# Kernel tuning notes

Hardware: AMD Instinct MI355X
Metric: run time of the kernel (lower is better)

## Reference

```python
import jax, jax.numpy as jnp
import numpy as np

T = 2048          # num tokens (single long prefill sequence)
HID = 2048        # hidden_size
NH = 16           # num query heads
NKV = 2           # num kv heads
HD = 128          # head_dim (kv_channels)
ROPE_BASE = 10000.0


def setup_inputs() -> dict:
    key = jax.random.key(0)
    k1, k2, k3, k4, k5 = jax.random.split(key, 5)
    s = 0.02
    return {
        "hidden_states": jax.random.normal(k1, (T, HID), dtype=jnp.float32),
        "positions": jnp.arange(T, dtype=jnp.int64 if jax.config.jax_enable_x64 else jnp.int32),
        "Wq": jax.random.normal(k2, (NH * HD, HID), dtype=jnp.float32) * s,
        "Wk": jax.random.normal(k3, (NKV * HD, HID), dtype=jnp.float32) * s,
        "Wv": jax.random.normal(k4, (NKV * HD, HID), dtype=jnp.float32) * s,
        "Wo": jax.random.normal(k5, (HID, NH * HD), dtype=jnp.float32) * s,
    }


def _rope_cos_sin(positions):
    # fp32 RoPE tables, HF-style (concat of freqs with itself)
    inv_freq = 1.0 / (ROPE_BASE ** (jnp.arange(0, HD, 2, dtype=jnp.float32) / HD))
    freqs = positions.astype(jnp.float32)[:, None] * inv_freq[None, :]   # [T, HD/2]
    emb = jnp.concatenate([freqs, freqs], axis=-1)                        # [T, HD]
    return jnp.cos(emb)[:, None, :], jnp.sin(emb)[:, None, :]             # [T,1,HD]


def _rotate_half(x):
    x1, x2 = jnp.split(x, 2, axis=-1)
    return jnp.concatenate([-x2, x1], axis=-1)


def reference(hidden_states, positions, Wq, Wk, Wv, Wo):
    dtype = hidden_states.dtype
    # fused QKV projection (weights concatenated once, single GEMM)
    W_fused = jnp.concatenate([Wq, Wk, Wv], axis=0)            # [q+2kv, HID]
    qkv = hidden_states @ W_fused.T                             # [T, q+2kv]
    q, k, v = jnp.split(qkv, [NH * HD, NH * HD + NKV * HD], axis=-1)

    # fp32 RoPE on q/k
    cos, sin = _rope_cos_sin(positions)                         # [T,1,HD]
    qf = q.reshape(T, NH, HD).astype(jnp.float32)
    kf = k.reshape(T, NKV, HD).astype(jnp.float32)
    qf = qf * cos + _rotate_half(qf) * sin
    kf = kf * cos + _rotate_half(kf) * sin
    q = qf.astype(dtype)                                        # [T,NH,HD]
    k = kf.astype(dtype)                                        # [T,NKV,HD]
    v = v.reshape(T, NKV, HD)

    # causal GQA attention (same math as the paged-attention kernel on one seq)
    group = NH // NKV
    k_rep = jnp.repeat(k, group, axis=1)                        # [T,NH,HD]
    v_rep = jnp.repeat(v, group, axis=1)                        # [T,NH,HD]
    scale = HD ** -0.5
    scores = jnp.einsum('qhd,khd->hqk', q, k_rep) * scale       # [NH,T,T]
    causal = jnp.tril(jnp.ones((T, T), dtype=bool))
    scores = jnp.where(causal[None], scores, jnp.finfo(scores.dtype).min)
    probs = jax.nn.softmax(scores, axis=-1)
    attn = jnp.einsum('hqk,khd->qhd', probs, v_rep).reshape(T, NH * HD)

    return attn @ Wo.T                                          # [T, HID]
```

## Files before the change

### kernel.cpp

```cpp
#include <hip/hip_runtime.h>

#define T_TOK 2048
#define HID   2048
#define NH    16
#define NKV   2
#define HD    128
#define QDIM  (NH * HD)
#define KVDIM (NKV * HD)
#define QKVDIM (QDIM + 2 * KVDIM)

typedef float          f32x4  __attribute__((ext_vector_type(4)));
typedef unsigned short u16x8  __attribute__((ext_vector_type(8)));
typedef __bf16         bf16x8 __attribute__((ext_vector_type(8)));

__device__ __forceinline__ unsigned short f2bf(float f) {
    __bf16 h = (__bf16)f;
    return __builtin_bit_cast(unsigned short, h);
}
__device__ __forceinline__ float bf2f(unsigned short u) {
    return (float)__builtin_bit_cast(__bf16, u);
}

__device__ __forceinline__ f32x4 mfma16(u16x8 a, u16x8 b, f32x4 c) {
    return __builtin_amdgcn_mfma_f32_16x16x32_bf16(
        __builtin_bit_cast(bf16x8, a), __builtin_bit_cast(bf16x8, b), c, 0, 0, 0);
}

#define QSCL 0.12751743f
#define DEFER_THR 11.5416f

__global__ __launch_bounds__(256) void pack_bf16_all(
    const float* __restrict__ hidden, const float* __restrict__ Wq,
    const float* __restrict__ Wk, const float* __restrict__ Wv,
    const float* __restrict__ Wo,
    unsigned short* __restrict__ hb, unsigned short* __restrict__ Wf,
    unsigned short* __restrict__ Wob)
{
    const int b = blockIdx.x;
    const float* src; unsigned short* dst; size_t off;
    if      (b < 2048) { src = hidden; dst = hb;            off = (size_t)b * 2048; }
    else if (b < 4096) { src = Wq;     dst = Wf;            off = (size_t)(b - 2048) * 2048; }
    else if (b < 4352) { src = Wk;     dst = Wf + 4194304;  off = (size_t)(b - 4096) * 2048; }
    else if (b < 4608) { src = Wv;     dst = Wf + 4718592;  off = (size_t)(b - 4352) * 2048; }
    else               { src = Wo;     dst = Wob;           off = (size_t)(b - 4608) * 2048; }

    const size_t i = off + threadIdx.x * 8;
    float4 f0 = *reinterpret_cast<const float4*>(src + i);
    float4 f1 = *reinterpret_cast<const float4*>(src + i + 4);
    u16x8 o;
    o[0]=f2bf(f0.x); o[1]=f2bf(f0.y); o[2]=f2bf(f0.z); o[3]=f2bf(f0.w);
    o[4]=f2bf(f1.x); o[5]=f2bf(f1.y); o[6]=f2bf(f1.z); o[7]=f2bf(f1.w);
    *reinterpret_cast<u16x8*>(dst + i) = o;
}

template<bool BF16OUT>
__global__ __launch_bounds__(256) void gemm_bf16(
    const unsigned short* __restrict__ A,
    const unsigned short* __restrict__ B,
    void* __restrict__ Cv,
    int K, int NC, int nbx)
{
    __shared__ alignas(16) unsigned short As[2][64 * 64];
    __shared__ alignas(16) unsigned short Bs[2][128 * 64];

    const int tid  = threadIdx.x;
    const int lane = tid & 63;
    const int w    = tid >> 6;
    const int lg   = lane >> 4, lc = lane & 15;

    const int cpx = gridDim.x >> 3;
    const int wg  = (blockIdx.x & 7) * cpx + (blockIdx.x >> 3);
    const int m0  = (wg / nbx) * 64, n0 = (wg % nbx) * 128;

    const int rowL = lane >> 3;
    const int gS   = (lane & 7) ^ rowL;
    const int wr   = (w >> 1) * 32, wc = (w & 1) * 64;

    f32x4 acc[2][4] = {};

    auto stage = [&](int buf, int kb) {
        #pragma unroll
        for (int ci = 0; ci < 2; ci++) {
            const int chunk = w * 2 + ci;
            const int row   = chunk * 8 + rowL;
            const unsigned short* gpA = &A[(size_t)(m0 + row) * K + kb + gS * 8];
            __builtin_amdgcn_global_load_lds(
                (const __attribute__((address_space(1))) void*)gpA,
                (__attribute__((address_space(3))) void*)(&As[buf][chunk * 512]),
                16, 0, 0);
        }
        #pragma unroll
        for (int ci = 0; ci < 4; ci++) {
            const int chunk = w * 4 + ci;
            const int row   = chunk * 8 + rowL;
            const unsigned short* gpB = &B[(size_t)(n0 + row) * K + kb + gS * 8];
            __builtin_amdgcn_global_load_lds(
                (const __attribute__((address_space(1))) void*)gpB,
                (__attribute__((address_space(3))) void*)(&Bs[buf][chunk * 512]),
                16, 0, 0);
        }
    };

    stage(0, 0);
    const int nk = K >> 6;
    for (int t = 0; t < nk; ++t) {
        if (t + 1 < nk) {
            stage((t + 1) & 1, (t + 1) * 64);
            asm volatile("s_waitcnt vmcnt(6)" ::: "memory");
        } else {
            asm volatile("s_waitcnt vmcnt(0)" ::: "memory");
        }
        __syncthreads();

        const unsigned short* As_ = As[t & 1];
        const unsigned short* Bs_ = Bs[t & 1];
        #pragma unroll
        for (int kk = 0; kk < 2; kk++) {
            u16x8 af[2], bf[4];
            const int g = (kk * 4 + lg) ^ (lc & 7);
            #pragma unroll
            for (int mi = 0; mi < 2; mi++) {
                const int r = wr + mi * 16 + lc;
                af[mi] = *reinterpret_cast<const u16x8*>(&As_[r * 64 + g * 8]);
            }
            #pragma unroll
            for (int ni = 0; ni < 4; ni++) {
                const int r = wc + ni * 16 + lc;
                bf[ni] = *reinterpret_cast<const u16x8*>(&Bs_[r * 64 + g * 8]);
            }
            #pragma unroll
            for (int mi = 0; mi < 2; mi++)
                #pragma unroll
                for (int ni = 0; ni < 4; ni++)
                    acc[mi][ni] = mfma16(af[mi], bf[ni], acc[mi][ni]);
        }
        __syncthreads();
    }

    #pragma unroll
    for (int mi = 0; mi < 2; mi++)
        #pragma unroll
        for (int ni = 0; ni < 4; ni++)
            #pragma unroll
            for (int j = 0; j < 4; j++) {
                const size_t idx = (size_t)(m0 + wr + mi * 16 + lg * 4 + j) * NC
                                   + n0 + wc + ni * 16 + lc;
                if constexpr (BF16OUT)
                    ((unsigned short*)Cv)[idx] = f2bf(acc[mi][ni][j]);
                else
                    ((float*)Cv)[idx] = acc[mi][ni][j];
            }
}

__global__ __launch_bounds__(256) void rope_vt(
    const unsigned short* __restrict__ qkvb,
    const int* __restrict__ positions,
    unsigned short* __restrict__ qr,
    unsigned short* __restrict__ kr,
    unsigned short* __restrict__ vt)
{
    __shared__ float cosv[64], sinv[64];
    __shared__ unsigned short tile[64][72];
    const int tid = threadIdx.x;

    if (blockIdx.x < 2048) {
        const int t = blockIdx.x;
        if (tid < 64) {
            float invf = expf(-(float)tid * 0.14391156831212787f);
            float f = (float)positions[t] * invf;
            cosv[tid] = cosf(f);
            sinv[tid] = sinf(f);
        }
        __syncthreads();

        const unsigned short* row = qkvb + (size_t)t * QKVDIM;
        for (int i = tid; i < NH * 64; i += 256) {
            int hh = i >> 6, j = i & 63;
            float x1 = bf2f(row[hh * HD + j]);
            float x2 = bf2f(row[hh * HD + j + 64]);
            float c = cosv[j], s = sinv[j];
            qr[(size_t)t * QDIM + hh * HD + j]      = f2bf((x1 * c - x2 * s) * QSCL);
            qr[(size_t)t * QDIM + hh * HD + j + 64] = f2bf((x2 * c + x1 * s) * QSCL);
        }
        if (tid < NKV * 64) {
            int hh = tid >> 6, j = tid & 63;
            float x1 = bf2f(row[QDIM + hh * HD + j]);
            float x2 = bf2f(row[QDIM + hh * HD + j + 64]);
            float c = cosv[j], s = sinv[j];
            kr[(size_t)t * KVDIM + hh * HD + j]      = f2bf(x1 * c - x2 * s);
            kr[(size_t)t * KVDIM + hh * HD + j + 64] = f2bf(x2 * c + x1 * s);
        }
    } else {
        const int bb = blockIdx.x - 2048;
        const int t0 = (bb & 31) * 64;
        const int d0 = (bb >> 5) * 64;
        {
            int r = tid >> 2;
            int c = (tid & 3) * 16;
            const unsigned short* src =
                &qkvb[(size_t)(t0 + r) * QKVDIM + QDIM + KVDIM + d0 + c];
            *reinterpret_cast<u16x8*>(&tile[r][c])     = *reinterpret_cast<const u16x8*>(src);
            *reinterpret_cast<u16x8*>(&tile[r][c + 8]) = *reinterpret_cast<const u16x8*>(src + 8);
        }
        __syncthreads();
        {
            int dr = tid >> 3;
            int tc = (tid & 7) * 8;
            #pragma unroll
            for (int i = 0; i < 2; i++) {
                int d = dr + i * 32;
                u16x8 ov;
                #pragma unroll
                for (int e = 0; e < 8; e++) ov[e] = tile[tc + e][d];
                *reinterpret_cast<u16x8*>(&vt[(size_t)(d0 + d) * T_TOK + t0 + tc]) = ov;
            }
        }
    }
}

__global__ __launch_bounds__(256) void attn_kernel(
    const unsigned short* __restrict__ q,
    const unsigned short* __restrict__ k,
    const unsigned short* __restrict__ vt,
    unsigned short* __restrict__ o,
    float* __restrict__ pO,
    float* __restrict__ pML)
{
    __shared__ alignas(16) unsigned short Ks[64 * 128];
    __shared__ alignas(16) unsigned short Vs[128 * 64];
    __shared__ alignas(16) unsigned short P[4][16][72];

    const int tid  = threadIdx.x;
    const int lane = tid & 63;
    const int w    = tid >> 6;
    const int lg   = lane >> 4, lc = lane & 15;
    const int b    = blockIdx.x;
    const int h    = b & 15;
    const int idx  = b >> 4;

    int tau, c0;
    if (idx <= 16)      { tau = 15 + idx; c0 = 0; }
    else if (idx == 17) { tau = 31;       c0 = 1; }
    else {
        int j = idx - 18, kk = 15 - (j >> 1);
        if ((j & 1) == 0) { tau = kk - 1;  c0 = 0; }
        else              { tau = kk + 15; c0 = 1; }
    }
    const int kstart = c0 << 4;
    const int kcnt   = min(16, tau + 1 - kstart);

    const int q0   = tau * 64 + w * 16;
    const int hk   = h >> 3;
    const int xr   = (lc & 7) << 4;

    const int krow_l = (lane >> 4);
    const int kgS    = (lane & 15);
    const int vrow_l = (lane >> 3);
    const int vgS    = (lane & 7);

    u16x8 qf[4];
    #pragma unroll
    for (int dc = 0; dc < 4; dc++)
        qf[dc] = *reinterpret_cast<const u16x8*>(
            &q[(size_t)(q0 + lc) * QDIM + h * HD + dc * 32 + lg * 8]);

    float mrow = -1e30f, ell = 0.f;
    f32x4 oacc[8] = {};

    auto stage = [&](int kb) {
        #pragma unroll
        for (int ci = 0; ci < 4; ci++) {
            const int chunk = w * 4 + ci;
            const int row   = chunk * 4 + krow_l;
            const int gSk   = kgS ^ (row & 7);
            const unsigned short* gp =
                &k[(size_t)(kb + row) * KVDIM + hk * HD + gSk * 8];
            __builtin_amdgcn_global_load_lds(
                (const __attribute__((address_space(1))) void*)gp,
                (__attribute__((address_space(3))) void*)(&Ks[chunk * 512]),
                16, 0, 0);
        }
        #pragma unroll
        for (int ci = 0; ci < 4; ci++) {
            const int chunk = w * 4 + ci;
            const int dr    = chunk * 8 + vrow_l;
            const int gSv   = vgS ^ (dr & 7);
            const unsigned short* gp =
                &vt[(size_t)(hk * HD + dr) * T_TOK + kb + gSv * 8];
            __builtin_amdgcn_global_load_lds(
                (const __attribute__((address_space(1))) void*)gp,
                (__attribute__((address_space(3))) void*)(&Vs[chunk * 512]),
                16, 0, 0);
        }
    };

    for (int it = 0; it < kcnt; ++it) {
        const int kb = (kstart + it) * 64;
        stage(kb);
        asm volatile("s_waitcnt vmcnt(4)" ::: "memory");
        __syncthreads();

        const char* KsB = (const char*)Ks;
        const char* VsB = (const char*)Vs;

        float sc[4][4];
        const bool dia = (kb + 63 > q0);
        #pragma unroll
        for (int c4 = 0; c4 < 4; c4++) {
            const int row = c4 * 16 + lc;
            f32x4 s = {0.f, 0.f, 0.f, 0.f};
            #pragma unroll
            for (int dc = 0; dc < 4; dc++) {
                u16x8 kf = *reinterpret_cast<const u16x8*>(
                    KsB + row * 256 + ((dc * 64 + lg * 16) ^ xr));
                s = mfma16(kf, qf[dc], s);
            }
            if (dia) {
                #pragma unroll
                for (int j = 0; j < 4; j++) {
                    const int kpos = kb + c4 * 16 + lg * 4 + j;
                    sc[c4][j] = (kpos <= q0 + lc) ? s[j] : -1e30f;
                }
            } else {
                #pragma unroll
                for (int j = 0; j < 4; j++) sc[c4][j] = s[j];
            }
        }

        float t01 = fmaxf(fmaxf(sc[0][0], sc[0][1]), fmaxf(sc[0][2], sc[0][3]));
        float t23 = fmaxf(fmaxf(sc[1][0], sc[1][1]), fmaxf(sc[1][2], sc[1][3]));
        float t45 = fmaxf(fmaxf(sc[2][0], sc[2][1]), fmaxf(sc[2][2], sc[2][3]));
        float t67 = fmaxf(fmaxf(sc[3][0], sc[3][1]), fmaxf(sc[3][2], sc[3][3]));
        float tmx = fmaxf(fmaxf(t01, t23), fmaxf(t45, t67));
        tmx = fmaxf(tmx, __shfl_xor(tmx, 16));
        tmx = fmaxf(tmx, __shfl_xor(tmx, 32));

        float mn;
        if (__all(tmx <= mrow + DEFER_THR)) {
            mn = mrow;
        } else {
            mn = fmaxf(mrow, tmx);
            float alpha = __builtin_amdgcn_exp2f(mrow - mn);
            mrow = mn;
            ell *= alpha;
            float aj[4];
            #pragma unroll
            for (int j = 0; j < 4; j++)
                aj[j] = __shfl(alpha, lg * 4 + j);
            #pragma unroll
            for (int d8 = 0; d8 < 8; d8++)
                #pragma unroll
                for (int j = 0; j < 4; j++)
                    oacc[d8][j] *= aj[j];
        }

        float rs = 0.f;
        #pragma unroll
        for (int c4 = 0; c4 < 4; c4++) {
            float p0 = __builtin_amdgcn_exp2f(sc[c4][0] - mn);
            float p1 = __builtin_amdgcn_exp2f(sc[c4][1] - mn);
            float p2 = __builtin_amdgcn_exp2f(sc[c4][2] - mn);
            float p3 = __builtin_amdgcn_exp2f(sc[c4][3] - mn);
            rs += (p0 + p1) + (p2 + p3);
            ushort4 pk;
            pk.x = f2bf(p0); pk.y = f2bf(p1); pk.z = f2bf(p2); pk.w = f2bf(p3);
            *reinterpret_cast<ushort4*>(&P[w][lc][c4 * 16 + lg * 4]) = pk;
        }
        rs += __shfl_xor(rs, 16);
        rs += __shfl_xor(rs, 32);
        ell += rs;

        asm volatile("s_waitcnt vmcnt(0) lgkmcnt(0)" ::: "memory");
        __builtin_amdgcn_sched_barrier(0);
        __syncthreads();

        u16x8 pf0 = *reinterpret_cast<const u16x8*>(&P[w][lc][lg * 8]);
        u16x8 pf1 = *reinterpret_cast<const u16x8*>(&P[w][lc][32 + lg * 8]);

        #pragma unroll
        for (int d8 = 0; d8 < 8; d8++) {
            const int drow = d8 * 16 + lc;
            u16x8 vf0 = *reinterpret_cast<const u16x8*>(
                VsB + drow * 128 + ((lg * 16) ^ xr));
            u16x8 vf1 = *reinterpret_cast<const u16x8*>(
                VsB + drow * 128 + ((lg * 16 + 64) ^ xr));
            oacc[d8] = mfma16(pf0, vf0, oacc[d8]);
            oacc[d8] = mfma16(pf1, vf1, oacc[d8]);
        }
        if (it + 1 < kcnt) __syncthreads();
    }

    if (tau < 16) {
        float ej[4];
        #pragma unroll
        for (int j = 0; j < 4; j++)
            ej[j] = __shfl(ell, lg * 4 + j);
        #pragma unroll
        for (int d8 = 0; d8 < 8; d8++)
            #pragma unroll
            for (int j = 0; j < 4; j++) {
                float val = oacc[d8][j] / ej[j];
                o[(size_t)(q0 + lg * 4 + j) * QDIM + h * HD + d8 * 16 + lc] = f2bf(val);
            }
    } else {
        const int s = (h * 16 + (tau - 16)) * 2 + c0;
        float* po = pO + (size_t)s * 8192;
        #pragma unroll
        for (int d8 = 0; d8 < 8; d8++)
            #pragma unroll
            for (int j = 0; j < 4; j++)
                po[(w * 16 + lg * 4 + j) * 128 + d8 * 16 + lc] = oacc[d8][j];
        if (lg == 0) {
            pML[s * 128 + w * 16 + lc]      = mrow;
            pML[s * 128 + 64 + w * 16 + lc] = ell;
        }
    }
}

__global__ __launch_bounds__(256) void attn_combine(
    const float* __restrict__ pO,
    const float* __restrict__ pML,
    unsigned short* __restrict__ o)
{
    const int b  = blockIdx.x;
    const int h  = b >> 4, ti = b & 15;
    const int tau = 16 + ti;
    const int s0 = (h * 16 + ti) * 2, s1 = s0 + 1;

    const int tid = threadIdx.x;
    const int r   = tid >> 2;
    const int cg  = (tid & 3) * 32;

    const float m1 = pML[s0 * 128 + r],      m2 = pML[s1 * 128 + r];
    const float l1 = pML[s0 * 128 + 64 + r], l2 = pML[s1 * 128 + 64 + r];
    const float M  = fmaxf(m1, m2);
    const float w1 = __builtin_amdgcn_exp2f(m1 - M);
    const float w2 = __builtin_amdgcn_exp2f(m2 - M);
    const float rn = 1.0f / (w1 * l1 + w2 * l2);

    const float* o1 = pO + (size_t)s0 * 8192 + r * 128 + cg;
    const float* o2 = pO + (size_t)s1 * 8192 + r * 128 + cg;
    unsigned short* dst = o + (size_t)(tau * 64 + r) * QDIM + h * HD + cg;

    #pragma unroll
    for (int i = 0; i < 8; i++) {
        float4 a = *reinterpret_cast<const float4*>(o1 + i * 4);
        float4 c = *reinterpret_cast<const float4*>(o2 + i * 4);
        ushort4 pk;
        pk.x = f2bf((w1 * a.x + w2 * c.x) * rn);
        pk.y = f2bf((w1 * a.y + w2 * c.y) * rn);
        pk.z = f2bf((w1 * a.z + w2 * c.z) * rn);
        pk.w = f2bf((w1 * a.w + w2 * c.w) * rn);
        *reinterpret_cast<ushort4*>(dst + i * 4) = pk;
    }
}

extern "C" void kernel_launch(void* const* d_in, const int* in_sizes, int n_in,
                              void* d_out, int out_size, void* d_ws, size_t ws_size,
                              hipStream_t stream) {
    const float* hidden    = (const float*)d_in[0];
    const int*   positions = (const int*)d_in[1];
    const float* Wq        = (const float*)d_in[2];
    const float* Wk        = (const float*)d_in[3];
    const float* Wv        = (const float*)d_in[4];
    const float* Wo        = (const float*)d_in[5];
    float*       out       = (float*)d_out;

    char* ws = (char*)d_ws;
    unsigned short* qkvb = (unsigned short*)(ws);
    unsigned short* qr  = (unsigned short*)(ws + 20971520);
    unsigned short* kr  = (unsigned short*)(ws + 29360128);
    unsigned short* vt  = (unsigned short*)(ws + 30408704);
    unsigned short* att = (unsigned short*)(ws + 31457280);
    unsigned short* hb  = (unsigned short*)(ws + 39845888);
    unsigned short* Wf  = (unsigned short*)(ws + 48234496);
    unsigned short* Wob = (unsigned short*)(ws + 58720256);
    float* pO  = (float*)(ws);
    float* pML = (float*)(ws + 16777216);

    pack_bf16_all<<<6656, 256, 0, stream>>>(hidden, Wq, Wk, Wv, Wo, hb, Wf, Wob);
    gemm_bf16<true><<<640, 256, 0, stream>>>(hb, Wf, qkvb, HID, QKVDIM, QKVDIM / 128);
    rope_vt<<<2176, 256, 0, stream>>>(qkvb, positions, qr, kr, vt);
    attn_kernel<<<NH * 48, 256, 0, stream>>>(qr, kr, vt, att, pO, pML);
    attn_combine<<<256, 256, 0, stream>>>(pO, pML, att);
    gemm_bf16<false><<<512, 256, 0, stream>>>(att, Wob, out, QDIM, HID, HID / 128);
}
```

Before: 130.3 us.

## Prefetch next K/V tile into registers while computing current attention tile

Replaces direct global-to-LDS loads with register-staged prefetch: the next tile's K and V are loaded into registers at the top of each iteration and written to LDS after the PV MFMAs. The goal is to hide global load latency behind the QK, softmax and PV compute instead of waiting on the loads at the start of every iteration. In exchange it adds register pressure (8 extra u16x8 per lane) and an extra barrier pair around the LDS write. It also removes the barrier between the P write and the P read, relying only on lgkmcnt for the per-wave P buffer.

```diff
diff --git a/kernel.cpp b/kernel.cpp
--- a/kernel.cpp
+++ b/kernel.cpp
@@ -267,38 +267,47 @@
     float mrow = -1e30f, ell = 0.f;
     f32x4 oacc[8] = {};
 
-    auto stage = [&](int kb) {
+    u16x8 kreg[4], vreg[4];
+
+    auto ldstage = [&](int kb) {
         #pragma unroll
         for (int ci = 0; ci < 4; ci++) {
             const int chunk = w * 4 + ci;
             const int row   = chunk * 4 + krow_l;
             const int gSk   = kgS ^ (row & 7);
-            const unsigned short* gp =
-                &k[(size_t)(kb + row) * KVDIM + hk * HD + gSk * 8];
-            __builtin_amdgcn_global_load_lds(
-                (const __attribute__((address_space(1))) void*)gp,
-                (__attribute__((address_space(3))) void*)(&Ks[chunk * 512]),
-                16, 0, 0);
+            kreg[ci] = *reinterpret_cast<const u16x8*>(
+                &k[(size_t)(kb + row) * KVDIM + hk * HD + gSk * 8]);
         }
         #pragma unroll
         for (int ci = 0; ci < 4; ci++) {
             const int chunk = w * 4 + ci;
             const int dr    = chunk * 8 + vrow_l;
             const int gSv   = vgS ^ (dr & 7);
-            const unsigned short* gp =
-                &vt[(size_t)(hk * HD + dr) * T_TOK + kb + gSv * 8];
-            __builtin_amdgcn_global_load_lds(
-                (const __attribute__((address_space(1))) void*)gp,
-                (__attribute__((address_space(3))) void*)(&Vs[chunk * 512]),
-                16, 0, 0);
+            vreg[ci] = *reinterpret_cast<const u16x8*>(
+                &vt[(size_t)(hk * HD + dr) * T_TOK + kb + gSv * 8]);
         }
     };
+    auto wrstage = [&]() {
+        #pragma unroll
+        for (int ci = 0; ci < 4; ci++) {
+            const int chunk = w * 4 + ci;
+            *reinterpret_cast<u16x8*>(&Ks[chunk * 512 + lane * 8]) = kreg[ci];
+        }
+        #pragma unroll
+        for (int ci = 0; ci < 4; ci++) {
+            const int chunk = w * 4 + ci;
+            *reinterpret_cast<u16x8*>(&Vs[chunk * 512 + lane * 8]) = vreg[ci];
+        }
+    };
+
+    ldstage(kstart * 64);
+    wrstage();
+    __syncthreads();
 
     for (int it = 0; it < kcnt; ++it) {
         const int kb = (kstart + it) * 64;
-        stage(kb);
-        asm volatile("s_waitcnt vmcnt(4)" ::: "memory");
-        __syncthreads();
+        if (it + 1 < kcnt)
+            ldstage((kstart + it + 1) * 64);
 
         const char* KsB = (const char*)Ks;
         const char* VsB = (const char*)Vs;
@@ -370,9 +379,8 @@
         rs += __shfl_xor(rs, 32);
         ell += rs;
 
-        asm volatile("s_waitcnt vmcnt(0) lgkmcnt(0)" ::: "memory");
+        asm volatile("s_waitcnt lgkmcnt(0)" ::: "memory");
         __builtin_amdgcn_sched_barrier(0);
-        __syncthreads();
 
         u16x8 pf0 = *reinterpret_cast<const u16x8*>(&P[w][lc][lg * 8]);
         u16x8 pf1 = *reinterpret_cast<const u16x8*>(&P[w][lc][32 + lg * 8]);
@@ -387,7 +395,12 @@
             oacc[d8] = mfma16(pf0, vf0, oacc[d8]);
             oacc[d8] = mfma16(pf1, vf1, oacc[d8]);
         }
-        if (it + 1 < kcnt) __syncthreads();
+
+        if (it + 1 < kcnt) {
+            __syncthreads();
+            wrstage();
+            __syncthreads();
+        }
     }
 
     if (tau < 16) {
```

Result: slower. 133.5 us (+2.5%).

## Fuse RoPE and V transpose into QKV GEMM epilogue

Applied to the files above, without the earlier changes.

Removes the separate rope_vt kernel by applying RoPE (with q scaling) to Q/K tiles in the QKV GEMM epilogue via an LDS staging buffer, and writing V directly transposed. Cos/sin tables are precomputed in extra blocks of the packing kernel. This avoids writing and re-reading the full bf16 QKV intermediate and one kernel launch, at the cost of extra shared memory, an epilogue sync, and strided transposed V stores.

```diff
diff --git a/kernel.cpp b/kernel.cpp
--- a/kernel.cpp
+++ b/kernel.cpp
@@ -17,9 +17,6 @@
     __bf16 h = (__bf16)f;
     return __builtin_bit_cast(unsigned short, h);
 }
-__device__ __forceinline__ float bf2f(unsigned short u) {
-    return (float)__builtin_bit_cast(__bf16, u);
-}
 
 __device__ __forceinline__ f32x4 mfma16(u16x8 a, u16x8 b, f32x4 c) {
     return __builtin_amdgcn_mfma_f32_16x16x32_bf16(
@@ -32,11 +29,21 @@
 __global__ __launch_bounds__(256) void pack_bf16_all(
     const float* __restrict__ hidden, const float* __restrict__ Wq,
     const float* __restrict__ Wk, const float* __restrict__ Wv,
-    const float* __restrict__ Wo,
+    const float* __restrict__ Wo, const int* __restrict__ positions,
     unsigned short* __restrict__ hb, unsigned short* __restrict__ Wf,
-    unsigned short* __restrict__ Wob)
+    unsigned short* __restrict__ Wob, float* __restrict__ ctab)
 {
     const int b = blockIdx.x;
+    if (b >= 6656) {
+        const int bb = b - 6656;
+        const int t  = bb * 4 + (threadIdx.x >> 6);
+        const int j  = threadIdx.x & 63;
+        float invf = expf(-(float)j * 0.14391156831212787f);
+        float f = (float)positions[t] * invf;
+        ctab[(size_t)t * 128 + j]      = cosf(f);
+        ctab[(size_t)t * 128 + 64 + j] = sinf(f);
+        return;
+    }
     const float* src; unsigned short* dst; size_t off;
     if      (b < 2048) { src = hidden; dst = hb;            off = (size_t)b * 2048; }
     else if (b < 4096) { src = Wq;     dst = Wf;            off = (size_t)(b - 2048) * 2048; }
@@ -53,21 +60,24 @@
     *reinterpret_cast<u16x8*>(dst + i) = o;
 }
 
-template<bool BF16OUT>
-__global__ __launch_bounds__(256) void gemm_bf16(
+__global__ __launch_bounds__(256) void qkv_gemm_fused(
     const unsigned short* __restrict__ A,
     const unsigned short* __restrict__ B,
-    void* __restrict__ Cv,
-    int K, int NC, int nbx)
+    const float* __restrict__ ctab,
+    unsigned short* __restrict__ qr,
+    unsigned short* __restrict__ kr,
+    unsigned short* __restrict__ vt)
 {
-    __shared__ alignas(16) unsigned short As[2][64 * 64];
-    __shared__ alignas(16) unsigned short Bs[2][128 * 64];
+    __shared__ alignas(16) char smem[49152];
+    unsigned short* AsBase = (unsigned short*)smem;
+    unsigned short* BsBase = (unsigned short*)(smem + 16384);
 
     const int tid  = threadIdx.x;
     const int lane = tid & 63;
     const int w    = tid >> 6;
     const int lg   = lane >> 4, lc = lane & 15;
 
+    const int nbx = QKVDIM / 128;
     const int cpx = gridDim.x >> 3;
     const int wg  = (blockIdx.x & 7) * cpx + (blockIdx.x >> 3);
     const int m0  = (wg / nbx) * 64, n0 = (wg % nbx) * 128;
@@ -83,26 +93,26 @@
         for (int ci = 0; ci < 2; ci++) {
             const int chunk = w * 2 + ci;
             const int row   = chunk * 8 + rowL;
-            const unsigned short* gpA = &A[(size_t)(m0 + row) * K + kb + gS * 8];
+            const unsigned short* gpA = &A[(size_t)(m0 + row) * HID + kb + gS * 8];
             __builtin_amdgcn_global_load_lds(
                 (const __attribute__((address_space(1))) void*)gpA,
-                (__attribute__((address_space(3))) void*)(&As[buf][chunk * 512]),
+                (__attribute__((address_space(3))) void*)(&AsBase[buf * 4096 + chunk * 512]),
                 16, 0, 0);
         }
         #pragma unroll
         for (int ci = 0; ci < 4; ci++) {
             const int chunk = w * 4 + ci;
             const int row   = chunk * 8 + rowL;
-            const unsigned short* gpB = &B[(size_t)(n0 + row) * K + kb + gS * 8];
+            const unsigned short* gpB = &B[(size_t)(n0 + row) * HID + kb + gS * 8];
             __builtin_amdgcn_global_load_lds(
                 (const __attribute__((address_space(1))) void*)gpB,
-                (__attribute__((address_space(3))) void*)(&Bs[buf][chunk * 512]),
+                (__attribute__((address_space(3))) void*)(&BsBase[buf * 8192 + chunk * 512]),
                 16, 0, 0);
         }
     };
 
     stage(0, 0);
-    const int nk = K >> 6;
+    const int nk = HID >> 6;
     for (int t = 0; t < nk; ++t) {
         if (t + 1 < nk) {
             stage((t + 1) & 1, (t + 1) * 64);
@@ -112,8 +122,8 @@
         }
         __syncthreads();
 
-        const unsigned short* As_ = As[t & 1];
-        const unsigned short* Bs_ = Bs[t & 1];
+        const unsigned short* As_ = &AsBase[(t & 1) * 4096];
+        const unsigned short* Bs_ = &BsBase[(t & 1) * 8192];
         #pragma unroll
         for (int kk = 0; kk < 2; kk++) {
             u16x8 af[2], bf[4];
@@ -137,85 +147,151 @@
         __syncthreads();
     }
 
+    if (n0 < QDIM + KVDIM) {
+        float* Ep = (float*)smem;
+        #pragma unroll
+        for (int mi = 0; mi < 2; mi++)
+            #pragma unroll
+            for (int ni = 0; ni < 4; ni++)
+                #pragma unroll
+                for (int j = 0; j < 4; j++)
+                    Ep[(wr + mi * 16 + lg * 4 + j) * 132 + wc + ni * 16 + lc]
+                        = acc[mi][ni][j];
+        __syncthreads();
+
+        const bool isq = (n0 < QDIM);
+        const float scl = isq ? QSCL : 1.0f;
+        unsigned short* dst  = isq ? qr : kr;
+        const int rowstride  = isq ? QDIM : KVDIM;
+        const int colbase    = isq ? n0 : (n0 - QDIM);
+
+        const int r  = tid >> 2;
+        const int jb = (tid & 3) * 16;
+        const float* ct = ctab + (size_t)(m0 + r) * 128;
+        unsigned short* drow = dst + (size_t)(m0 + r) * rowstride + colbase;
+        #pragma unroll
+        for (int g = 0; g < 4; g++) {
+            ushort4 p1, p2;
+            #pragma unroll
+            for (int e = 0; e < 4; e++) {
+                const int j = jb + g * 4 + e;
+                float x1 = Ep[r * 132 + j];
+                float x2 = Ep[r * 132 + j + 64];
+                float c = ct[j], s = ct[64 + j];
+                ((unsigned short*)&p1)[e] = f2bf((x1 * c - x2 * s) * scl);
+                ((unsigned short*)&p2)[e] = f2bf((x2 * c + x1 * s) * scl);
+            }
+            *reinterpret_cast<ushort4*>(drow + jb + g * 4)      = p1;
+            *reinterpret_cast<ushort4*>(drow + jb + g * 4 + 64) = p2;
+        }
+    } else {
+        #pragma unroll
+        for (int mi = 0; mi < 2; mi++)
+            #pragma unroll
+            for (int ni = 0; ni < 4; ni++) {
+                const int d   = (n0 - QDIM - KVDIM) + wc + ni * 16 + lc;
+                const int t0r = m0 + wr + mi * 16 + lg * 4;
+                ushort4 pk;
+                pk.x = f2bf(acc[mi][ni][0]);
+                pk.y = f2bf(acc[mi][ni][1]);
+                pk.z = f2bf(acc[mi][ni][2]);
+                pk.w = f2bf(acc[mi][ni][3]);
+                *reinterpret_cast<ushort4*>(&vt[(size_t)d * T_TOK + t0r]) = pk;
+            }
+    }
+}
+
+__global__ __launch_bounds__(256) void gemm_out(
+    const unsigned short* __restrict__ A,
+    const unsigned short* __restrict__ B,
+    float* __restrict__ C)
+{
+    __shared__ alignas(16) unsigned short As[2][64 * 64];
+    __shared__ alignas(16) unsigned short Bs[2][128 * 64];
+
+    const int tid  = threadIdx.x;
+    const int lane = tid & 63;
+    const int w    = tid >> 6;
+    const int lg   = lane >> 4, lc = lane & 15;
+
+    const int nbx = HID / 128;
+    const int cpx = gridDim.x >> 3;
+    const int wg  = (blockIdx.x & 7) * cpx + (blockIdx.x >> 3);
+    const int m0  = (wg / nbx) * 64, n0 = (wg % nbx) * 128;
+
+    const int rowL = lane >> 3;
+    const int gS   = (lane & 7) ^ rowL;
+    const int wr   = (w >> 1) * 32, wc = (w & 1) * 64;
+
+    f32x4 acc[2][4] = {};
+
+    auto stage = [&](int buf, int kb) {
+        #pragma unroll
+        for (int ci = 0; ci < 2; ci++) {
+            const int chunk = w * 2 + ci;
+            const int row   = chunk * 8 + rowL;
+            const unsigned short* gpA = &A[(size_t)(m0 + row) * QDIM + kb + gS * 8];
+            __builtin_amdgcn_global_load_lds(
+                (const __attribute__((address_space(1))) void*)gpA,
+                (__attribute__((address_space(3))) void*)(&As[buf][chunk * 512]),
+                16, 0, 0);
+        }
+        #pragma unroll
+        for (int ci = 0; ci < 4; ci++) {
+            const int chunk = w * 4 + ci;
+            const int row   = chunk * 8 + rowL;
+            const unsigned short* gpB = &B[(size_t)(n0 + row) * QDIM + kb + gS * 8];
+            __builtin_amdgcn_global_load_lds(
+                (const __attribute__((address_space(1))) void*)gpB,
+                (__attribute__((address_space(3))) void*)(&Bs[buf][chunk * 512]),
+                16, 0, 0);
+        }
+    };
+
+    stage(0, 0);
+    const int nk = QDIM >> 6;
+    for (int t = 0; t < nk; ++t) {
+        if (t + 1 < nk) {
+            stage((t + 1) & 1, (t + 1) * 64);
+            asm volatile("s_waitcnt vmcnt(6)" ::: "memory");
+        } else {
+            asm volatile("s_waitcnt vmcnt(0)" ::: "memory");
+        }
+        __syncthreads();
+
+        const unsigned short* As_ = As[t & 1];
+        const unsigned short* Bs_ = Bs[t & 1];
+        #pragma unroll
+        for (int kk = 0; kk < 2; kk++) {
+            u16x8 af[2], bf[4];
+            const int g = (kk * 4 + lg) ^ (lc & 7);
+            #pragma unroll
+            for (int mi = 0; mi < 2; mi++) {
+                const int r = wr + mi * 16 + lc;
+                af[mi] = *reinterpret_cast<const u16x8*>(&As_[r * 64 + g * 8]);
+            }
+            #pragma unroll
+            for (int ni = 0; ni < 4; ni++) {
+                const int r = wc + ni * 16 + lc;
+                bf[ni] = *reinterpret_cast<const u16x8*>(&Bs_[r * 64 + g * 8]);
+            }
+            #pragma unroll
+            for (int mi = 0; mi < 2; mi++)
+                #pragma unroll
+                for (int ni = 0; ni < 4; ni++)
+                    acc[mi][ni] = mfma16(af[mi], bf[ni], acc[mi][ni]);
+        }
+        __syncthreads();
+    }
+
     #pragma unroll
     for (int mi = 0; mi < 2; mi++)
         #pragma unroll
         for (int ni = 0; ni < 4; ni++)
             #pragma unroll
-            for (int j = 0; j < 4; j++) {
-                const size_t idx = (size_t)(m0 + wr + mi * 16 + lg * 4 + j) * NC
-                                   + n0 + wc + ni * 16 + lc;
-                if constexpr (BF16OUT)
-                    ((unsigned short*)Cv)[idx] = f2bf(acc[mi][ni][j]);
-                else
-                    ((float*)Cv)[idx] = acc[mi][ni][j];
-            }
-}
-
-__global__ __launch_bounds__(256) void rope_vt(
-    const unsigned short* __restrict__ qkvb,
-    const int* __restrict__ positions,
-    unsigned short* __restrict__ qr,
-    unsigned short* __restrict__ kr,
-    unsigned short* __restrict__ vt)
-{
-    __shared__ float cosv[64], sinv[64];
-    __shared__ unsigned short tile[64][72];
-    const int tid = threadIdx.x;
-
-    if (blockIdx.x < 2048) {
-        const int t = blockIdx.x;
-        if (tid < 64) {
-            float invf = expf(-(float)tid * 0.14391156831212787f);
-            float f = (float)positions[t] * invf;
-            cosv[tid] = cosf(f);
-            sinv[tid] = sinf(f);
-        }
-        __syncthreads();
-
-        const unsigned short* row = qkvb + (size_t)t * QKVDIM;
-        for (int i = tid; i < NH * 64; i += 256) {
-            int hh = i >> 6, j = i & 63;
-            float x1 = bf2f(row[hh * HD + j]);
-            float x2 = bf2f(row[hh * HD + j + 64]);
-            float c = cosv[j], s = sinv[j];
-            qr[(size_t)t * QDIM + hh * HD + j]      = f2bf((x1 * c - x2 * s) * QSCL);
-            qr[(size_t)t * QDIM + hh * HD + j + 64] = f2bf((x2 * c + x1 * s) * QSCL);
-        }
-        if (tid < NKV * 64) {
-            int hh = tid >> 6, j = tid & 63;
-            float x1 = bf2f(row[QDIM + hh * HD + j]);
-            float x2 = bf2f(row[QDIM + hh * HD + j + 64]);
-            float c = cosv[j], s = sinv[j];
-            kr[(size_t)t * KVDIM + hh * HD + j]      = f2bf(x1 * c - x2 * s);
-            kr[(size_t)t * KVDIM + hh * HD + j + 64] = f2bf(x2 * c + x1 * s);
-        }
-    } else {
-        const int bb = blockIdx.x - 2048;
-        const int t0 = (bb & 31) * 64;
-        const int d0 = (bb >> 5) * 64;
-        {
-            int r = tid >> 2;
-            int c = (tid & 3) * 16;
-            const unsigned short* src =
-                &qkvb[(size_t)(t0 + r) * QKVDIM + QDIM + KVDIM + d0 + c];
-            *reinterpret_cast<u16x8*>(&tile[r][c])     = *reinterpret_cast<const u16x8*>(src);
-            *reinterpret_cast<u16x8*>(&tile[r][c + 8]) = *reinterpret_cast<const u16x8*>(src + 8);
-        }
-        __syncthreads();
-        {
-            int dr = tid >> 3;
-            int tc = (tid & 7) * 8;
-            #pragma unroll
-            for (int i = 0; i < 2; i++) {
-                int d = dr + i * 32;
-                u16x8 ov;
-                #pragma unroll
-                for (int e = 0; e < 8; e++) ov[e] = tile[tc + e][d];
-                *reinterpret_cast<u16x8*>(&vt[(size_t)(d0 + d) * T_TOK + t0 + tc]) = ov;
-            }
-        }
-    }
+            for (int j = 0; j < 4; j++)
+                C[(size_t)(m0 + wr + mi * 16 + lg * 4 + j) * HID
+                  + n0 + wc + ni * 16 + lc] = acc[mi][ni][j];
 }
 
 __global__ __launch_bounds__(256) void attn_kernel(
@@ -467,7 +543,9 @@
     float*       out       = (float*)d_out;
 
     char* ws = (char*)d_ws;
-    unsigned short* qkvb = (unsigned short*)(ws);
+    float* pO   = (float*)(ws);
+    float* pML  = (float*)(ws + 16777216);
+    float* ctab = (float*)(ws + 17039360);
     unsigned short* qr  = (unsigned short*)(ws + 20971520);
     unsigned short* kr  = (unsigned short*)(ws + 29360128);
     unsigned short* vt  = (unsigned short*)(ws + 30408704);
@@ -475,13 +553,11 @@
     unsigned short* hb  = (unsigned short*)(ws + 39845888);
     unsigned short* Wf  = (unsigned short*)(ws + 48234496);
     unsigned short* Wob = (unsigned short*)(ws + 58720256);
-    float* pO  = (float*)(ws);
-    float* pML = (float*)(ws + 16777216);
-
-    pack_bf16_all<<<6656, 256, 0, stream>>>(hidden, Wq, Wk, Wv, Wo, hb, Wf, Wob);
-    gemm_bf16<true><<<640, 256, 0, stream>>>(hb, Wf, qkvb, HID, QKVDIM, QKVDIM / 128);
-    rope_vt<<<2176, 256, 0, stream>>>(qkvb, positions, qr, kr, vt);
+
+    pack_bf16_all<<<7168, 256, 0, stream>>>(hidden, Wq, Wk, Wv, Wo, positions,
+                                            hb, Wf, Wob, ctab);
+    qkv_gemm_fused<<<640, 256, 0, stream>>>(hb, Wf, ctab, qr, kr, vt);
     attn_kernel<<<NH * 48, 256, 0, stream>>>(qr, kr, vt, att, pO, pML);
     attn_combine<<<256, 256, 0, stream>>>(pO, pML, att);
-    gemm_bf16<false><<<512, 256, 0, stream>>>(att, Wob, out, QDIM, HID, HID / 128);
-}
+    gemm_out<<<512, 256, 0, stream>>>(att, Wob, out);
+}
```

Result: no change. 127.9 us (-1.8%).
